# Kernel optimization log

Hardware: AMD Instinct MI355X
Metric: run time of the kernel (lower is better)

Reference implementation:

```python
import jax, jax.numpy as jnp
import numpy as np

N_ATOMS, N_NBH, N_IN, N_FILTERS, N_OUT, N_GAUSS = 10000, 48, 128, 128, 128, 25
R_CUTOFF = 5.0
LOG2 = float(np.log(2.0))


def ssp(v):
    # shifted softplus, the SchNet activation
    return jax.nn.softplus(v) - LOG2


def setup_inputs() -> dict:
    key = jax.random.key(0)
    ks = jax.random.split(key, 10)
    x = jax.random.normal(ks[0], (N_ATOMS, N_IN), dtype=jnp.float32)
    dR = jax.random.uniform(ks[1], (N_ATOMS, N_NBH), dtype=jnp.float32) * 10.0  # distances in [0,10)
    dR_expanded = jax.random.normal(ks[2], (N_ATOMS, N_NBH, N_GAUSS), dtype=jnp.float32)
    pairwise_mask = jnp.ones((N_ATOMS, N_NBH), dtype=jnp.float32)
    neighbors_idx = jax.random.randint(ks[3], (N_ATOMS, N_NBH), 0, N_ATOMS, dtype=jnp.int32)
    s = 1.0 / np.sqrt(N_FILTERS)
    W1 = jax.random.normal(ks[4], (N_GAUSS, N_FILTERS), dtype=jnp.float32) * (1.0 / np.sqrt(N_GAUSS))
    b1 = jnp.zeros((N_FILTERS,), dtype=jnp.float32)
    W2 = jax.random.normal(ks[5], (N_FILTERS, N_FILTERS), dtype=jnp.float32) * s
    b2 = jnp.zeros((N_FILTERS,), dtype=jnp.float32)
    W_in2f = jax.random.normal(ks[6], (N_IN, N_FILTERS), dtype=jnp.float32) * (1.0 / np.sqrt(N_IN))
    W_f2out = jax.random.normal(ks[7], (N_FILTERS, N_OUT), dtype=jnp.float32) * s
    b_f2out = jnp.zeros((N_OUT,), dtype=jnp.float32)
    return {"x": x, "dR": dR, "dR_expanded": dR_expanded, "pairwise_mask": pairwise_mask,
            "neighbors_idx": neighbors_idx, "W1": W1, "b1": b1, "W2": W2, "b2": b2,
            "W_in2f": W_in2f, "W_f2out": W_f2out, "b_f2out": b_f2out}


def reference(x, dR, dR_expanded, pairwise_mask, neighbors_idx,
              W1, b1, W2, b2, W_in2f, W_f2out, b_f2out):
    # FilterNetwork: Dense + ssp + Dense, on Gaussian-smeared distances -> [N, K, F]
    W = jnp.einsum('nkg,gf->nkf', dR_expanded, W1) + b1
    W = jnp.einsum('nkf,fh->nkh', ssp(W), W2) + b2
    # HardCutoff: 1 where within cutoff
    C = (dR <= R_CUTOFF).astype(W.dtype)           # [N, K]
    W = W * C[..., None]
    # in2f (no bias), gather neighbor features
    y = x @ W_in2f                                  # [N, F]
    y = jnp.take(y, neighbors_idx, axis=0)          # [N, K, F] (gather == take_along_axis path)
    # filter-weighted multiply + masked sum aggregation over neighbor axis
    y = y * W
    y = jnp.sum(y * pairwise_mask[..., None], axis=1)  # [N, F]
    # f2out: Linear + shifted softplus
    return ssp(y @ W_f2out + b_f2out)               # [N, n_out]
```

## Files before the change

### kernel.cpp

```cpp
#include <hip/hip_runtime.h>
#include <hip/hip_bf16.h>


#define NA 10000
#define NK 48
#define NF 128
#define HP  136
#define YFP 136
#define GRID_CF 1024

typedef __bf16 bf16x8 __attribute__((ext_vector_type(8)));
typedef float  f32x4  __attribute__((ext_vector_type(4)));

__device__ __forceinline__ unsigned short f2bs(float x) {
    return __builtin_bit_cast(unsigned short, (__bf16)x);
}
__device__ __forceinline__ float bs2f(unsigned short u) {
    return (float)__builtin_bit_cast(__bf16, u);
}
__device__ __forceinline__ float sspf(float v) {
    return fmaxf(v, 0.0f) + __logf(1.0f + __expf(-fabsf(v))) - 0.69314718056f;
}

__global__ __launch_bounds__(256) void in2f_prep(
    const float* __restrict__ x,
    const float* __restrict__ Wi,
    const float* __restrict__ W1,
    const float* __restrict__ W2,
    const float* __restrict__ Wo,
    const float* __restrict__ dRe,
    unsigned short* __restrict__ wsb,
    unsigned short* __restrict__ yfeatb,
    unsigned short* __restrict__ dreb)
{
    const int tid = threadIdx.x;

    if (blockIdx.x >= 301) {
        const float4* src = (const float4*)dRe;
        for (int j = (blockIdx.x - 301) * 256 + tid; j < 3000000; j += 768 * 256) {
            float4 v = src[j];
            int n  = j / 300;
            int rm = j - n * 300;
            int i  = rm * 4;
            int k  = i / 25;
            int g  = i - k * 25;
            unsigned short* dst = dreb + (size_t)n * 1536;
            float vv[4] = {v.x, v.y, v.z, v.w};
            #pragma unroll
            for (int e = 0; e < 4; ++e) {
                dst[k * 32 + g] = f2bs(vv[e]);
                if (++g == 25) {
                    #pragma unroll
                    for (int p = 25; p < 32; ++p) dst[k * 32 + p] = 0;
                    g = 0; ++k;
                }
            }
        }
        return;
    }

    if (blockIdx.x >= 157) {
        int i = (blockIdx.x - 157) * 256 + tid;
        if (i < 4096) {
            int f = i >> 5, g = i & 31;
            wsb[i] = (g < 25) ? f2bs(W1[g * NF + f]) : (unsigned short)0;
        } else if (i < 20480) {
            int j = i - 4096; int h = j >> 7, k = j & 127;
            wsb[i] = f2bs(W2[k * NF + h]);
        } else {
            int j = i - 20480; int f = j >> 7, k = j & 127;
            wsb[i] = f2bs(Wo[k * NF + f]);
        }
        return;
    }

    __shared__ __align__(16) unsigned short s_wi[NF * 136];
    {
        const float4* wi4 = (const float4*)Wi;
        #pragma unroll
        for (int it = 0; it < 16; ++it) {
            int idx4 = it * 256 + tid;
            float4 v = wi4[idx4];
            int i = idx4 >> 5;
            int f = (idx4 & 31) * 4;
            s_wi[(f + 0) * 136 + i] = f2bs(v.x);
            s_wi[(f + 1) * 136 + i] = f2bs(v.y);
            s_wi[(f + 2) * 136 + i] = f2bs(v.z);
            s_wi[(f + 3) * 136 + i] = f2bs(v.w);
        }
    }
    __syncthreads();

    const int w = tid >> 6;
    const int lane = tid & 63;
    const int r = lane & 15;
    const int q = lane >> 4;
    const int m0 = blockIdx.x * 64 + w * 16;
    const int row = m0 + r;
    const bool rv = (row < NA);

    f32x4 acc[8];
    #pragma unroll
    for (int nt = 0; nt < 8; ++nt) { acc[nt][0]=0.f; acc[nt][1]=0.f; acc[nt][2]=0.f; acc[nt][3]=0.f; }

    #pragma unroll
    for (int ks = 0; ks < 4; ++ks) {
        bf16x8 a;
        if (rv) {
            const float4* xp = (const float4*)(x + (size_t)row * NF + ks * 32 + q * 8);
            float4 v0 = xp[0], v1 = xp[1];
            a[0]=(__bf16)v0.x; a[1]=(__bf16)v0.y; a[2]=(__bf16)v0.z; a[3]=(__bf16)v0.w;
            a[4]=(__bf16)v1.x; a[5]=(__bf16)v1.y; a[6]=(__bf16)v1.z; a[7]=(__bf16)v1.w;
        } else {
            #pragma unroll
            for (int j = 0; j < 8; ++j) a[j] = (__bf16)0.0f;
        }
        #pragma unroll
        for (int nt = 0; nt < 8; ++nt) {
            bf16x8 b = *(const bf16x8*)(&s_wi[(nt * 16 + r) * 136 + ks * 32 + q * 8]);
            acc[nt] = __builtin_amdgcn_mfma_f32_16x16x32_bf16(a, b, acc[nt], 0, 0, 0);
        }
    }
    #pragma unroll
    for (int nt = 0; nt < 8; ++nt) {
        #pragma unroll
        for (int reg = 0; reg < 4; ++reg) {
            int orow = m0 + q * 4 + reg;
            if (orow < NA)
                yfeatb[(size_t)orow * NF + nt * 16 + r] = f2bs(acc[nt][reg]);
        }
    }
}

__global__ __launch_bounds__(256, 4) void cfconv_pp(
    const float* __restrict__ dR,
    const float* __restrict__ mask,
    const int*   __restrict__ nbr,
    const float* __restrict__ b1,
    const float* __restrict__ b2,
    const unsigned short* __restrict__ W1T,
    const unsigned short* __restrict__ W2T,
    const unsigned short* __restrict__ dreb,
    const unsigned short* __restrict__ yfeatb,
    float* __restrict__ yout)
{
    __shared__ __align__(16) unsigned short s_H[NK * HP];
    __shared__ __align__(16) unsigned short s_yf[NK * YFP];
    __shared__ float s_cm[NK];

    const int tid = threadIdx.x;
    const int w = tid >> 6;
    const int lane = tid & 63;
    const int r = lane & 15;
    const int q = lane >> 4;
    const int nt0 = w * 2;
    const int kb = tid >> 4;
    const int sp = tid & 15;

    const bf16x8 bfr0 = *(const bf16x8*)(W1T + ((nt0    ) * 16 + r) * 32 + q * 8);
    const bf16x8 bfr1 = *(const bf16x8*)(W1T + ((nt0 + 1) * 16 + r) * 32 + q * 8);
    bf16x8 bw[2][4];
    #pragma unroll
    for (int t = 0; t < 2; ++t)
        #pragma unroll
        for (int ks = 0; ks < 4; ++ks)
            bw[t][ks] = *(const bf16x8*)(W2T + ((nt0 + t) * 16 + r) * NF + ks * 32 + q * 8);
    const float bias1a = b1[nt0 * 16 + r];
    const float bias1b = b1[nt0 * 16 + 16 + r];
    const float bias2a = b2[nt0 * 16 + r];
    const float bias2b = b2[nt0 * 16 + 16 + r];

    bf16x8 g0, g1, g2;
    bf16x8 a0, a1, a2;
    float dv = 10.0f, mv = 0.0f;
    unsigned short hsv[24];

    auto prefetch = [&](int nn) {
        const int nb0 = nbr[nn * NK + kb] * NF;
        const int nb1 = nbr[nn * NK + kb + 16] * NF;
        const int nb2 = nbr[nn * NK + kb + 32] * NF;
        g0 = *(const bf16x8*)(yfeatb + nb0 + sp * 8);
        g1 = *(const bf16x8*)(yfeatb + nb1 + sp * 8);
        g2 = *(const bf16x8*)(yfeatb + nb2 + sp * 8);
        const unsigned short* dn = dreb + (size_t)nn * 1536;
        a0 = *(const bf16x8*)(dn + (     r) * 32 + q * 8);
        a1 = *(const bf16x8*)(dn + (16 + r) * 32 + q * 8);
        a2 = *(const bf16x8*)(dn + (32 + r) * 32 + q * 8);
        if (tid < NK) {
            dv = dR[nn * NK + tid];
            mv = mask[nn * NK + tid];
        }
    };

    auto stage1 = [&]() {
        #pragma unroll
        for (int mt = 0; mt < 3; ++mt) {
            bf16x8 av8 = (mt == 0) ? a0 : (mt == 1) ? a1 : a2;
            f32x4 zf; zf[0]=0.f; zf[1]=0.f; zf[2]=0.f; zf[3]=0.f;
            f32x4 h0v = __builtin_amdgcn_mfma_f32_16x16x32_bf16(av8, bfr0, zf, 0, 0, 0);
            f32x4 h1v = __builtin_amdgcn_mfma_f32_16x16x32_bf16(av8, bfr1, zf, 0, 0, 0);
            #pragma unroll
            for (int reg = 0; reg < 4; ++reg) {
                hsv[mt * 8 + reg]     = f2bs(sspf(h0v[reg] + bias1a));
                hsv[mt * 8 + 4 + reg] = f2bs(sspf(h1v[reg] + bias1b));
            }
        }
    };

    auto ldswrite = [&]() {
        #pragma unroll
        for (int mt = 0; mt < 3; ++mt) {
            #pragma unroll
            for (int reg = 0; reg < 4; ++reg) {
                int k = mt * 16 + q * 4 + reg;
                s_H[k * HP + nt0 * 16 + r]      = hsv[mt * 8 + reg];
                s_H[k * HP + nt0 * 16 + 16 + r] = hsv[mt * 8 + 4 + reg];
            }
        }
        *(bf16x8*)(&s_yf[(kb     ) * YFP + sp * 8]) = g0;
        *(bf16x8*)(&s_yf[(kb + 16) * YFP + sp * 8]) = g1;
        *(bf16x8*)(&s_yf[(kb + 32) * YFP + sp * 8]) = g2;
        if (tid < NK)
            s_cm[tid] = (dv <= 5.0f) ? mv : 0.0f;
    };

    int n = blockIdx.x;
    prefetch(n);
    stage1();
    ldswrite();
    __syncthreads();

    while (true) {
        const int n_next = n + GRID_CF;
        const bool more = (n_next < NA);

        if (more) prefetch(n_next);

        f32x4 acc[3][2];
        #pragma unroll
        for (int mt = 0; mt < 3; ++mt)
            #pragma unroll
            for (int t = 0; t < 2; ++t) { acc[mt][t][0]=0.f; acc[mt][t][1]=0.f; acc[mt][t][2]=0.f; acc[mt][t][3]=0.f; }

        #pragma unroll
        for (int ks = 0; ks < 4; ++ks) {
            #pragma unroll
            for (int mt = 0; mt < 3; ++mt) {
                bf16x8 ah = *(const bf16x8*)(&s_H[(mt * 16 + r) * HP + ks * 32 + q * 8]);
                acc[mt][0] = __builtin_amdgcn_mfma_f32_16x16x32_bf16(ah, bw[0][ks], acc[mt][0], 0, 0, 0);
                acc[mt][1] = __builtin_amdgcn_mfma_f32_16x16x32_bf16(ah, bw[1][ks], acc[mt][1], 0, 0, 0);
            }
        }

        if (more) stage1();

        float part0 = 0.f, part1 = 0.f;
        const int h0 = nt0 * 16 + r;
        #pragma unroll
        for (int mt = 0; mt < 3; ++mt) {
            #pragma unroll
            for (int reg = 0; reg < 4; ++reg) {
                int k = mt * 16 + q * 4 + reg;
                float cmk = s_cm[k];
                part0 += cmk * (acc[mt][0][reg] + bias2a) * bs2f(s_yf[k * YFP + h0]);
                part1 += cmk * (acc[mt][1][reg] + bias2b) * bs2f(s_yf[k * YFP + h0 + 16]);
            }
        }
        part0 += __shfl_xor(part0, 16);
        part0 += __shfl_xor(part0, 32);
        part1 += __shfl_xor(part1, 16);
        part1 += __shfl_xor(part1, 32);
        if (q == 0) {
            yout[(size_t)n * NF + h0]      = part0;
            yout[(size_t)n * NF + h0 + 16] = part1;
        }

        if (!more) break;

        __syncthreads();
        ldswrite();
        __syncthreads();
        n = n_next;
    }
}

__global__ __launch_bounds__(256) void f2out_mfma(
    const unsigned short* __restrict__ WoT,
    const float* __restrict__ bo,
    float* io)
{
    const int tid = threadIdx.x;
    const int w = tid >> 6;
    const int lane = tid & 63;
    const int r = lane & 15;
    const int q = lane >> 4;
    const int m0 = blockIdx.x * 64 + w * 16;
    const int row = m0 + r;
    const bool rv = (row < NA);

    f32x4 acc[8];
    #pragma unroll
    for (int nt = 0; nt < 8; ++nt) { acc[nt][0]=0.f; acc[nt][1]=0.f; acc[nt][2]=0.f; acc[nt][3]=0.f; }

    #pragma unroll
    for (int ks = 0; ks < 4; ++ks) {
        bf16x8 a;
        if (rv) {
            const float4* yp = (const float4*)(io + (size_t)row * NF + ks * 32 + q * 8);
            float4 v0 = yp[0], v1 = yp[1];
            a[0]=(__bf16)v0.x; a[1]=(__bf16)v0.y; a[2]=(__bf16)v0.z; a[3]=(__bf16)v0.w;
            a[4]=(__bf16)v1.x; a[5]=(__bf16)v1.y; a[6]=(__bf16)v1.z; a[7]=(__bf16)v1.w;
        } else {
            #pragma unroll
            for (int j = 0; j < 8; ++j) a[j] = (__bf16)0.0f;
        }
        #pragma unroll
        for (int nt = 0; nt < 8; ++nt) {
            bf16x8 b = *(const bf16x8*)(WoT + (nt * 16 + r) * NF + ks * 32 + q * 8);
            acc[nt] = __builtin_amdgcn_mfma_f32_16x16x32_bf16(a, b, acc[nt], 0, 0, 0);
        }
    }
    #pragma unroll
    for (int nt = 0; nt < 8; ++nt) {
        float bia = bo[nt * 16 + r];
        #pragma unroll
        for (int reg = 0; reg < 4; ++reg) {
            int orow = m0 + q * 4 + reg;
            if (orow < NA)
                io[(size_t)orow * NF + nt * 16 + r] = sspf(acc[nt][reg] + bia);
        }
    }
}

extern "C" void kernel_launch(void* const* d_in, const int* in_sizes, int n_in,
                              void* d_out, int out_size, void* d_ws, size_t ws_size,
                              hipStream_t stream)
{
    const float* x    = (const float*)d_in[0];
    const float* dR   = (const float*)d_in[1];
    const float* dRe  = (const float*)d_in[2];
    const float* mask = (const float*)d_in[3];
    const int*   nbr  = (const int*)d_in[4];
    const float* W1   = (const float*)d_in[5];
    const float* b1   = (const float*)d_in[6];
    const float* W2   = (const float*)d_in[7];
    const float* b2   = (const float*)d_in[8];
    const float* Wi2f = (const float*)d_in[9];
    const float* Wf2o = (const float*)d_in[10];
    const float* bf2o = (const float*)d_in[11];
    float* out = (float*)d_out;

    unsigned short* wsb = (unsigned short*)d_ws;
    unsigned short* W1T    = wsb;
    unsigned short* W2T    = wsb + 4096;
    unsigned short* WoT    = wsb + 20480;
    unsigned short* yfeatb = wsb + 36864;
    unsigned short* dreb   = wsb + 1316864;

    in2f_prep<<<1069, 256, 0, stream>>>(x, Wi2f, W1, W2, Wf2o, dRe,
                                        wsb, yfeatb, dreb);
    cfconv_pp<<<GRID_CF, 256, 0, stream>>>(dR, mask, nbr, b1, b2,
                                           W1T, W2T, dreb, yfeatb, out);
    f2out_mfma<<<157, 256, 0, stream>>>(WoT, bf2o, out);
}
```

Baseline: 209.5 us.

## Fuse prep, cfconv and f2out into one persistent kernel with grid barriers

Merges the three launches (weight/dR_expanded conversion plus in2f GEMM, the cfconv filter/aggregation loop, and the f2out GEMM) into a single persistent kernel. Phases are separated by software grid barriers built on atomic counters, and the grid is sized from the occupancy query (up to 6 blocks per CU × 256). The aim is to remove launch gaps and tail effects between kernels. In exchange it adds barrier spin costs, a memset launch, and a deadlock risk if the grid is not fully co-resident; the old three-kernel path is kept as a fallback when the workspace is too small.

```diff
diff --git a/kernel.cpp b/kernel.cpp
--- a/kernel.cpp
+++ b/kernel.cpp
@@ -7,7 +7,6 @@
 #define NF 128
 #define HP  136
 #define YFP 136
-#define GRID_CF 1024
 
 typedef __bf16 bf16x8 __attribute__((ext_vector_type(8)));
 typedef float  f32x4  __attribute__((ext_vector_type(4)));
@@ -22,7 +21,311 @@
     return fmaxf(v, 0.0f) + __logf(1.0f + __expf(-fabsf(v))) - 0.69314718056f;
 }
 
-__global__ __launch_bounds__(256) void in2f_prep(
+__device__ __forceinline__ void gridbar(unsigned int* cnt, unsigned int target) {
+    __syncthreads();
+    if (threadIdx.x == 0) {
+        __threadfence();
+        __hip_atomic_fetch_add(cnt, 1u, __ATOMIC_ACQ_REL, __HIP_MEMORY_SCOPE_AGENT);
+        unsigned int guard = 0;
+        while (__hip_atomic_load(cnt, __ATOMIC_ACQUIRE, __HIP_MEMORY_SCOPE_AGENT) < target) {
+            if (++guard > 100000000u) break;
+            __builtin_amdgcn_s_sleep(2);
+        }
+        __threadfence();
+    }
+    __syncthreads();
+}
+
+__global__ __launch_bounds__(256, 4) void cfconv_fused(
+    const float* __restrict__ x,
+    const float* __restrict__ dR,
+    const float* __restrict__ dRe,
+    const float* __restrict__ mask,
+    const int*   __restrict__ nbr,
+    const float* __restrict__ b1,
+    const float* __restrict__ b2,
+    const float* __restrict__ W1,
+    const float* __restrict__ W2,
+    const float* __restrict__ Wi,
+    const float* __restrict__ Wo,
+    const float* __restrict__ bf2o,
+    unsigned short* __restrict__ wsb,
+    unsigned short* __restrict__ yfeatb,
+    unsigned short* __restrict__ dreb,
+    unsigned int* bar,
+    float* __restrict__ out)
+{
+    __shared__ __align__(16) unsigned short s_H[NK * HP];
+    __shared__ __align__(16) unsigned short s_yf[NK * YFP];
+    __shared__ float s_cm[NK];
+
+    const int tid  = threadIdx.x;
+    const int bid  = blockIdx.x;
+    const int nblk = gridDim.x;
+    const unsigned int NB = (unsigned int)nblk;
+
+    const int w = tid >> 6;
+    const int lane = tid & 63;
+    const int r = lane & 15;
+    const int q = lane >> 4;
+    const int nt0 = w * 2;
+    const int kb = tid >> 4;
+    const int sp = tid & 15;
+
+    const unsigned short* W1T = wsb;
+    const unsigned short* W2T = wsb + 4096;
+    const unsigned short* WiT = wsb + 20480;
+    const unsigned short* WoT = wsb + 36864;
+
+    {
+        int i = bid * 256 + tid;
+        if (i < 4096) {
+            int f = i >> 5, g = i & 31;
+            wsb[i] = (g < 25) ? f2bs(W1[g * NF + f]) : (unsigned short)0;
+        } else if (i < 20480) {
+            int j = i - 4096; int h = j >> 7, k = j & 127;
+            wsb[i] = f2bs(W2[k * NF + h]);
+        } else if (i < 36864) {
+            int j = i - 20480; int f = j >> 7, k = j & 127;
+            wsb[i] = f2bs(Wi[k * NF + f]);
+        } else if (i < 53248) {
+            int j = i - 36864; int f = j >> 7, k = j & 127;
+            wsb[i] = f2bs(Wo[k * NF + f]);
+        }
+
+        const float4* src = (const float4*)dRe;
+        for (int j = bid * 256 + tid; j < 3000000; j += nblk * 256) {
+            float4 v = src[j];
+            int n  = j / 300;
+            int rm = j - n * 300;
+            int i2 = rm * 4;
+            int k  = i2 / 25;
+            int g  = i2 - k * 25;
+            unsigned short* dst = dreb + (size_t)n * 1536;
+            float vv[4] = {v.x, v.y, v.z, v.w};
+            #pragma unroll
+            for (int e = 0; e < 4; ++e) {
+                dst[k * 32 + g] = f2bs(vv[e]);
+                if (++g == 25) {
+                    #pragma unroll
+                    for (int p = 25; p < 32; ++p) dst[k * 32 + p] = 0;
+                    g = 0; ++k;
+                }
+            }
+        }
+    }
+    gridbar(bar + 0, NB);
+
+    for (int tile = bid; tile < 157; tile += nblk) {
+        const int m0 = tile * 64 + w * 16;
+        const int row = m0 + r;
+        const bool rv = (row < NA);
+
+        f32x4 acc[8];
+        #pragma unroll
+        for (int nt = 0; nt < 8; ++nt) { acc[nt][0]=0.f; acc[nt][1]=0.f; acc[nt][2]=0.f; acc[nt][3]=0.f; }
+
+        #pragma unroll
+        for (int ks = 0; ks < 4; ++ks) {
+            bf16x8 a;
+            if (rv) {
+                const float4* xp = (const float4*)(x + (size_t)row * NF + ks * 32 + q * 8);
+                float4 v0 = xp[0], v1 = xp[1];
+                a[0]=(__bf16)v0.x; a[1]=(__bf16)v0.y; a[2]=(__bf16)v0.z; a[3]=(__bf16)v0.w;
+                a[4]=(__bf16)v1.x; a[5]=(__bf16)v1.y; a[6]=(__bf16)v1.z; a[7]=(__bf16)v1.w;
+            } else {
+                #pragma unroll
+                for (int j = 0; j < 8; ++j) a[j] = (__bf16)0.0f;
+            }
+            #pragma unroll
+            for (int nt = 0; nt < 8; ++nt) {
+                bf16x8 b = *(const bf16x8*)(WiT + (nt * 16 + r) * NF + ks * 32 + q * 8);
+                acc[nt] = __builtin_amdgcn_mfma_f32_16x16x32_bf16(a, b, acc[nt], 0, 0, 0);
+            }
+        }
+        #pragma unroll
+        for (int nt = 0; nt < 8; ++nt) {
+            #pragma unroll
+            for (int reg = 0; reg < 4; ++reg) {
+                int orow = m0 + q * 4 + reg;
+                if (orow < NA)
+                    yfeatb[(size_t)orow * NF + nt * 16 + r] = f2bs(acc[nt][reg]);
+            }
+        }
+    }
+    gridbar(bar + 1, NB);
+
+    {
+        const bf16x8 bfr0 = *(const bf16x8*)(W1T + ((nt0    ) * 16 + r) * 32 + q * 8);
+        const bf16x8 bfr1 = *(const bf16x8*)(W1T + ((nt0 + 1) * 16 + r) * 32 + q * 8);
+        bf16x8 bw[2][4];
+        #pragma unroll
+        for (int t = 0; t < 2; ++t)
+            #pragma unroll
+            for (int ks = 0; ks < 4; ++ks)
+                bw[t][ks] = *(const bf16x8*)(W2T + ((nt0 + t) * 16 + r) * NF + ks * 32 + q * 8);
+        const float bias1a = b1[nt0 * 16 + r];
+        const float bias1b = b1[nt0 * 16 + 16 + r];
+        const float bias2a = b2[nt0 * 16 + r];
+        const float bias2b = b2[nt0 * 16 + 16 + r];
+
+        bf16x8 g0, g1, g2;
+        bf16x8 a0, a1, a2;
+        float dv = 10.0f, mv = 0.0f;
+        unsigned short hsv[24];
+
+        auto prefetch = [&](int nn) {
+            const int nb0 = nbr[nn * NK + kb] * NF;
+            const int nb1 = nbr[nn * NK + kb + 16] * NF;
+            const int nb2 = nbr[nn * NK + kb + 32] * NF;
+            g0 = *(const bf16x8*)(yfeatb + nb0 + sp * 8);
+            g1 = *(const bf16x8*)(yfeatb + nb1 + sp * 8);
+            g2 = *(const bf16x8*)(yfeatb + nb2 + sp * 8);
+            const unsigned short* dn = dreb + (size_t)nn * 1536;
+            a0 = *(const bf16x8*)(dn + (     r) * 32 + q * 8);
+            a1 = *(const bf16x8*)(dn + (16 + r) * 32 + q * 8);
+            a2 = *(const bf16x8*)(dn + (32 + r) * 32 + q * 8);
+            if (tid < NK) {
+                dv = dR[nn * NK + tid];
+                mv = mask[nn * NK + tid];
+            }
+        };
+
+        auto stage1 = [&]() {
+            #pragma unroll
+            for (int mt = 0; mt < 3; ++mt) {
+                bf16x8 av8 = (mt == 0) ? a0 : (mt == 1) ? a1 : a2;
+                f32x4 zf; zf[0]=0.f; zf[1]=0.f; zf[2]=0.f; zf[3]=0.f;
+                f32x4 h0v = __builtin_amdgcn_mfma_f32_16x16x32_bf16(av8, bfr0, zf, 0, 0, 0);
+                f32x4 h1v = __builtin_amdgcn_mfma_f32_16x16x32_bf16(av8, bfr1, zf, 0, 0, 0);
+                #pragma unroll
+                for (int reg = 0; reg < 4; ++reg) {
+                    hsv[mt * 8 + reg]     = f2bs(sspf(h0v[reg] + bias1a));
+                    hsv[mt * 8 + 4 + reg] = f2bs(sspf(h1v[reg] + bias1b));
+                }
+            }
+        };
+
+        auto ldswrite = [&]() {
+            #pragma unroll
+            for (int mt = 0; mt < 3; ++mt) {
+                #pragma unroll
+                for (int reg = 0; reg < 4; ++reg) {
+                    int k = mt * 16 + q * 4 + reg;
+                    s_H[k * HP + nt0 * 16 + r]      = hsv[mt * 8 + reg];
+                    s_H[k * HP + nt0 * 16 + 16 + r] = hsv[mt * 8 + 4 + reg];
+                }
+            }
+            *(bf16x8*)(&s_yf[(kb     ) * YFP + sp * 8]) = g0;
+            *(bf16x8*)(&s_yf[(kb + 16) * YFP + sp * 8]) = g1;
+            *(bf16x8*)(&s_yf[(kb + 32) * YFP + sp * 8]) = g2;
+            if (tid < NK)
+                s_cm[tid] = (dv <= 5.0f) ? mv : 0.0f;
+        };
+
+        int n = bid;
+        prefetch(n);
+        stage1();
+        ldswrite();
+        __syncthreads();
+
+        while (true) {
+            const int n_next = n + nblk;
+            const bool more = (n_next < NA);
+
+            if (more) prefetch(n_next);
+
+            f32x4 acc[3][2];
+            #pragma unroll
+            for (int mt = 0; mt < 3; ++mt)
+                #pragma unroll
+                for (int t = 0; t < 2; ++t) { acc[mt][t][0]=0.f; acc[mt][t][1]=0.f; acc[mt][t][2]=0.f; acc[mt][t][3]=0.f; }
+
+            #pragma unroll
+            for (int ks = 0; ks < 4; ++ks) {
+                #pragma unroll
+                for (int mt = 0; mt < 3; ++mt) {
+                    bf16x8 ah = *(const bf16x8*)(&s_H[(mt * 16 + r) * HP + ks * 32 + q * 8]);
+                    acc[mt][0] = __builtin_amdgcn_mfma_f32_16x16x32_bf16(ah, bw[0][ks], acc[mt][0], 0, 0, 0);
+                    acc[mt][1] = __builtin_amdgcn_mfma_f32_16x16x32_bf16(ah, bw[1][ks], acc[mt][1], 0, 0, 0);
+                }
+            }
+
+            if (more) stage1();
+
+            float part0 = 0.f, part1 = 0.f;
+            const int h0 = nt0 * 16 + r;
+            #pragma unroll
+            for (int mt = 0; mt < 3; ++mt) {
+                #pragma unroll
+                for (int reg = 0; reg < 4; ++reg) {
+                    int k = mt * 16 + q * 4 + reg;
+                    float cmk = s_cm[k];
+                    part0 += cmk * (acc[mt][0][reg] + bias2a) * bs2f(s_yf[k * YFP + h0]);
+                    part1 += cmk * (acc[mt][1][reg] + bias2b) * bs2f(s_yf[k * YFP + h0 + 16]);
+                }
+            }
+            part0 += __shfl_xor(part0, 16);
+            part0 += __shfl_xor(part0, 32);
+            part1 += __shfl_xor(part1, 16);
+            part1 += __shfl_xor(part1, 32);
+            if (q == 0) {
+                out[(size_t)n * NF + h0]      = part0;
+                out[(size_t)n * NF + h0 + 16] = part1;
+            }
+
+            if (!more) break;
+
+            __syncthreads();
+            ldswrite();
+            __syncthreads();
+            n = n_next;
+        }
+    }
+    gridbar(bar + 2, NB);
+
+    for (int tile = bid; tile < 157; tile += nblk) {
+        const int m0 = tile * 64 + w * 16;
+        const int row = m0 + r;
+        const bool rv = (row < NA);
+
+        f32x4 acc[8];
+        #pragma unroll
+        for (int nt = 0; nt < 8; ++nt) { acc[nt][0]=0.f; acc[nt][1]=0.f; acc[nt][2]=0.f; acc[nt][3]=0.f; }
+
+        #pragma unroll
+        for (int ks = 0; ks < 4; ++ks) {
+            bf16x8 a;
+            if (rv) {
+                const float4* yp = (const float4*)(out + (size_t)row * NF + ks * 32 + q * 8);
+                float4 v0 = yp[0], v1 = yp[1];
+                a[0]=(__bf16)v0.x; a[1]=(__bf16)v0.y; a[2]=(__bf16)v0.z; a[3]=(__bf16)v0.w;
+                a[4]=(__bf16)v1.x; a[5]=(__bf16)v1.y; a[6]=(__bf16)v1.z; a[7]=(__bf16)v1.w;
+            } else {
+                #pragma unroll
+                for (int j = 0; j < 8; ++j) a[j] = (__bf16)0.0f;
+            }
+            #pragma unroll
+            for (int nt = 0; nt < 8; ++nt) {
+                bf16x8 b = *(const bf16x8*)(WoT + (nt * 16 + r) * NF + ks * 32 + q * 8);
+                acc[nt] = __builtin_amdgcn_mfma_f32_16x16x32_bf16(a, b, acc[nt], 0, 0, 0);
+            }
+        }
+        #pragma unroll
+        for (int nt = 0; nt < 8; ++nt) {
+            float bia = bf2o[nt * 16 + r];
+            #pragma unroll
+            for (int reg = 0; reg < 4; ++reg) {
+                int orow = m0 + q * 4 + reg;
+                if (orow < NA)
+                    out[(size_t)orow * NF + nt * 16 + r] = sspf(acc[nt][reg] + bia);
+            }
+        }
+    }
+}
+
+
+__global__ __launch_bounds__(256) void in2f_prep_fb(
     const float* __restrict__ x,
     const float* __restrict__ Wi,
     const float* __restrict__ W1,
@@ -132,7 +435,7 @@
     }
 }
 
-__global__ __launch_bounds__(256, 4) void cfconv_pp(
+__global__ __launch_bounds__(256, 4) void cfconv_pp_fb(
     const float* __restrict__ dR,
     const float* __restrict__ mask,
     const int*   __restrict__ nbr,
@@ -170,8 +473,7 @@
     const float bias2a = b2[nt0 * 16 + r];
     const float bias2b = b2[nt0 * 16 + 16 + r];
 
-    bf16x8 g0, g1, g2;
-    bf16x8 a0, a1, a2;
+    bf16x8 g0, g1, g2, a0, a1, a2;
     float dv = 10.0f, mv = 0.0f;
     unsigned short hsv[24];
 
@@ -186,12 +488,8 @@
         a0 = *(const bf16x8*)(dn + (     r) * 32 + q * 8);
         a1 = *(const bf16x8*)(dn + (16 + r) * 32 + q * 8);
         a2 = *(const bf16x8*)(dn + (32 + r) * 32 + q * 8);
-        if (tid < NK) {
-            dv = dR[nn * NK + tid];
-            mv = mask[nn * NK + tid];
-        }
+        if (tid < NK) { dv = dR[nn * NK + tid]; mv = mask[nn * NK + tid]; }
     };
-
     auto stage1 = [&]() {
         #pragma unroll
         for (int mt = 0; mt < 3; ++mt) {
@@ -206,34 +504,28 @@
             }
         }
     };
-
     auto ldswrite = [&]() {
         #pragma unroll
-        for (int mt = 0; mt < 3; ++mt) {
+        for (int mt = 0; mt < 3; ++mt)
             #pragma unroll
             for (int reg = 0; reg < 4; ++reg) {
                 int k = mt * 16 + q * 4 + reg;
                 s_H[k * HP + nt0 * 16 + r]      = hsv[mt * 8 + reg];
                 s_H[k * HP + nt0 * 16 + 16 + r] = hsv[mt * 8 + 4 + reg];
             }
-        }
         *(bf16x8*)(&s_yf[(kb     ) * YFP + sp * 8]) = g0;
         *(bf16x8*)(&s_yf[(kb + 16) * YFP + sp * 8]) = g1;
         *(bf16x8*)(&s_yf[(kb + 32) * YFP + sp * 8]) = g2;
-        if (tid < NK)
-            s_cm[tid] = (dv <= 5.0f) ? mv : 0.0f;
+        if (tid < NK) s_cm[tid] = (dv <= 5.0f) ? mv : 0.0f;
     };
 
     int n = blockIdx.x;
-    prefetch(n);
-    stage1();
-    ldswrite();
+    prefetch(n); stage1(); ldswrite();
     __syncthreads();
 
     while (true) {
-        const int n_next = n + GRID_CF;
+        const int n_next = n + 1024;
         const bool more = (n_next < NA);
-
         if (more) prefetch(n_next);
 
         f32x4 acc[3][2];
@@ -243,21 +535,20 @@
             for (int t = 0; t < 2; ++t) { acc[mt][t][0]=0.f; acc[mt][t][1]=0.f; acc[mt][t][2]=0.f; acc[mt][t][3]=0.f; }
 
         #pragma unroll
-        for (int ks = 0; ks < 4; ++ks) {
+        for (int ks = 0; ks < 4; ++ks)
             #pragma unroll
             for (int mt = 0; mt < 3; ++mt) {
                 bf16x8 ah = *(const bf16x8*)(&s_H[(mt * 16 + r) * HP + ks * 32 + q * 8]);
                 acc[mt][0] = __builtin_amdgcn_mfma_f32_16x16x32_bf16(ah, bw[0][ks], acc[mt][0], 0, 0, 0);
                 acc[mt][1] = __builtin_amdgcn_mfma_f32_16x16x32_bf16(ah, bw[1][ks], acc[mt][1], 0, 0, 0);
             }
-        }
 
         if (more) stage1();
 
         float part0 = 0.f, part1 = 0.f;
         const int h0 = nt0 * 16 + r;
         #pragma unroll
-        for (int mt = 0; mt < 3; ++mt) {
+        for (int mt = 0; mt < 3; ++mt)
             #pragma unroll
             for (int reg = 0; reg < 4; ++reg) {
                 int k = mt * 16 + q * 4 + reg;
@@ -265,7 +556,6 @@
                 part0 += cmk * (acc[mt][0][reg] + bias2a) * bs2f(s_yf[k * YFP + h0]);
                 part1 += cmk * (acc[mt][1][reg] + bias2b) * bs2f(s_yf[k * YFP + h0 + 16]);
             }
-        }
         part0 += __shfl_xor(part0, 16);
         part0 += __shfl_xor(part0, 32);
         part1 += __shfl_xor(part1, 16);
@@ -276,7 +566,6 @@
         }
 
         if (!more) break;
-
         __syncthreads();
         ldswrite();
         __syncthreads();
@@ -284,7 +573,7 @@
     }
 }
 
-__global__ __launch_bounds__(256) void f2out_mfma(
+__global__ __launch_bounds__(256) void f2out_mfma_fb(
     const unsigned short* __restrict__ WoT,
     const float* __restrict__ bo,
     float* io)
@@ -351,15 +640,36 @@
     float* out = (float*)d_out;
 
     unsigned short* wsb = (unsigned short*)d_ws;
-    unsigned short* W1T    = wsb;
-    unsigned short* W2T    = wsb + 4096;
-    unsigned short* WoT    = wsb + 20480;
-    unsigned short* yfeatb = wsb + 36864;
-    unsigned short* dreb   = wsb + 1316864;
-
-    in2f_prep<<<1069, 256, 0, stream>>>(x, Wi2f, W1, W2, Wf2o, dRe,
-                                        wsb, yfeatb, dreb);
-    cfconv_pp<<<GRID_CF, 256, 0, stream>>>(dR, mask, nbr, b1, b2,
-                                           W1T, W2T, dreb, yfeatb, out);
-    f2out_mfma<<<157, 256, 0, stream>>>(WoT, bf2o, out);
-}
+
+    bool fused_ok = ws_size >= 33386752ULL;
+    int occ = 0;
+    if (fused_ok) {
+        if (hipOccupancyMaxActiveBlocksPerMultiprocessor(&occ, cfconv_fused, 256, 0) != hipSuccess)
+            occ = 0;
+        if (occ < 1) fused_ok = false;
+    }
+
+    if (fused_ok) {
+        unsigned short* yfb  = wsb + 53248;
+        unsigned short* dreb = wsb + 1333248;
+        unsigned int*   bar  = (unsigned int*)(wsb + 16693248);
+        int bpc  = occ > 6 ? 6 : occ;
+        int grid = bpc * 256;
+        if (grid > 1536) grid = 1536;
+        hipMemsetAsync(bar, 0, 128, stream);
+        cfconv_fused<<<grid, 256, 0, stream>>>(x, dR, dRe, mask, nbr, b1, b2,
+                                               W1, W2, Wi2f, Wf2o, bf2o,
+                                               wsb, yfb, dreb, bar, out);
+    } else {
+        unsigned short* W1T    = wsb;
+        unsigned short* W2T    = wsb + 4096;
+        unsigned short* WoT    = wsb + 20480;
+        unsigned short* yfeatb = wsb + 36864;
+        unsigned short* dreb   = wsb + 1316864;
+        in2f_prep_fb<<<1069, 256, 0, stream>>>(x, Wi2f, W1, W2, Wf2o, dRe,
+                                               wsb, yfeatb, dreb);
+        cfconv_pp_fb<<<1024, 256, 0, stream>>>(dR, mask, nbr, b1, b2,
+                                               W1T, W2T, dreb, yfeatb, out);
+        f2out_mfma_fb<<<157, 256, 0, stream>>>(WoT, bf2o, out);
+    }
+}
```

Measured after the change: 571.0 us. 173% more time.

## Read fp32 Gaussian expansion directly in cfconv instead of bf16 pre-pass

Applied to the files above, without the earlier changes.

Drops the separate pass that converted dR_expanded to a padded bf16 buffer. The cfconv kernel now loads the fp32 values straight from the input and converts them to bf16 in registers. Lanes with q==3 load only the 25th element and zero-fill the rest of the padded K. Weight transposes move into their own small kernel, and in2f reads a pre-transposed Wi from global memory instead of building it in LDS. This removes about 48MB of write-plus-reread traffic, at the cost of unaligned fp32 loads inside the main kernel and one extra kernel launch.

```diff
diff --git a/kernel.cpp b/kernel.cpp
--- a/kernel.cpp
+++ b/kernel.cpp
@@ -22,75 +22,35 @@
     return fmaxf(v, 0.0f) + __logf(1.0f + __expf(-fabsf(v))) - 0.69314718056f;
 }
 
-__global__ __launch_bounds__(256) void in2f_prep(
-    const float* __restrict__ x,
-    const float* __restrict__ Wi,
+__global__ __launch_bounds__(256) void prep_weights(
     const float* __restrict__ W1,
     const float* __restrict__ W2,
+    const float* __restrict__ Wi,
     const float* __restrict__ Wo,
-    const float* __restrict__ dRe,
-    unsigned short* __restrict__ wsb,
-    unsigned short* __restrict__ yfeatb,
-    unsigned short* __restrict__ dreb)
+    unsigned short* __restrict__ wsb)
+{
+    int i = blockIdx.x * 256 + threadIdx.x;
+    if (i < 4096) {
+        int f = i >> 5, g = i & 31;
+        wsb[i] = (g < 25) ? f2bs(W1[g * NF + f]) : (unsigned short)0;
+    } else if (i < 20480) {
+        int j = i - 4096; int h = j >> 7, k = j & 127;
+        wsb[i] = f2bs(W2[k * NF + h]);
+    } else if (i < 36864) {
+        int j = i - 20480; int f = j >> 7, k = j & 127;
+        wsb[i] = f2bs(Wi[k * NF + f]);
+    } else if (i < 53248) {
+        int j = i - 36864; int f = j >> 7, k = j & 127;
+        wsb[i] = f2bs(Wo[k * NF + f]);
+    }
+}
+
+__global__ __launch_bounds__(256) void in2f_mfma(
+    const float* __restrict__ x,
+    const unsigned short* __restrict__ WiT,
+    unsigned short* __restrict__ yfeatb)
 {
     const int tid = threadIdx.x;
-
-    if (blockIdx.x >= 301) {
-        const float4* src = (const float4*)dRe;
-        for (int j = (blockIdx.x - 301) * 256 + tid; j < 3000000; j += 768 * 256) {
-            float4 v = src[j];
-            int n  = j / 300;
-            int rm = j - n * 300;
-            int i  = rm * 4;
-            int k  = i / 25;
-            int g  = i - k * 25;
-            unsigned short* dst = dreb + (size_t)n * 1536;
-            float vv[4] = {v.x, v.y, v.z, v.w};
-            #pragma unroll
-            for (int e = 0; e < 4; ++e) {
-                dst[k * 32 + g] = f2bs(vv[e]);
-                if (++g == 25) {
-                    #pragma unroll
-                    for (int p = 25; p < 32; ++p) dst[k * 32 + p] = 0;
-                    g = 0; ++k;
-                }
-            }
-        }
-        return;
-    }
-
-    if (blockIdx.x >= 157) {
-        int i = (blockIdx.x - 157) * 256 + tid;
-        if (i < 4096) {
-            int f = i >> 5, g = i & 31;
-            wsb[i] = (g < 25) ? f2bs(W1[g * NF + f]) : (unsigned short)0;
-        } else if (i < 20480) {
-            int j = i - 4096; int h = j >> 7, k = j & 127;
-            wsb[i] = f2bs(W2[k * NF + h]);
-        } else {
-            int j = i - 20480; int f = j >> 7, k = j & 127;
-            wsb[i] = f2bs(Wo[k * NF + f]);
-        }
-        return;
-    }
-
-    __shared__ __align__(16) unsigned short s_wi[NF * 136];
-    {
-        const float4* wi4 = (const float4*)Wi;
-        #pragma unroll
-        for (int it = 0; it < 16; ++it) {
-            int idx4 = it * 256 + tid;
-            float4 v = wi4[idx4];
-            int i = idx4 >> 5;
-            int f = (idx4 & 31) * 4;
-            s_wi[(f + 0) * 136 + i] = f2bs(v.x);
-            s_wi[(f + 1) * 136 + i] = f2bs(v.y);
-            s_wi[(f + 2) * 136 + i] = f2bs(v.z);
-            s_wi[(f + 3) * 136 + i] = f2bs(v.w);
-        }
-    }
-    __syncthreads();
-
     const int w = tid >> 6;
     const int lane = tid & 63;
     const int r = lane & 15;
@@ -117,7 +77,7 @@
         }
         #pragma unroll
         for (int nt = 0; nt < 8; ++nt) {
-            bf16x8 b = *(const bf16x8*)(&s_wi[(nt * 16 + r) * 136 + ks * 32 + q * 8]);
+            bf16x8 b = *(const bf16x8*)(WiT + (nt * 16 + r) * NF + ks * 32 + q * 8);
             acc[nt] = __builtin_amdgcn_mfma_f32_16x16x32_bf16(a, b, acc[nt], 0, 0, 0);
         }
     }
@@ -132,15 +92,15 @@
     }
 }
 
-__global__ __launch_bounds__(256, 4) void cfconv_pp(
+__global__ __launch_bounds__(256, 4) void cfconv_ppd(
     const float* __restrict__ dR,
+    const float* __restrict__ dRe,
     const float* __restrict__ mask,
     const int*   __restrict__ nbr,
     const float* __restrict__ b1,
     const float* __restrict__ b2,
     const unsigned short* __restrict__ W1T,
     const unsigned short* __restrict__ W2T,
-    const unsigned short* __restrict__ dreb,
     const unsigned short* __restrict__ yfeatb,
     float* __restrict__ yout)
 {
@@ -171,7 +131,7 @@
     const float bias2b = b2[nt0 * 16 + 16 + r];
 
     bf16x8 g0, g1, g2;
-    bf16x8 a0, a1, a2;
+    float  fv[3][8];
     float dv = 10.0f, mv = 0.0f;
     unsigned short hsv[24];
 
@@ -182,10 +142,16 @@
         g0 = *(const bf16x8*)(yfeatb + nb0 + sp * 8);
         g1 = *(const bf16x8*)(yfeatb + nb1 + sp * 8);
         g2 = *(const bf16x8*)(yfeatb + nb2 + sp * 8);
-        const unsigned short* dn = dreb + (size_t)nn * 1536;
-        a0 = *(const bf16x8*)(dn + (     r) * 32 + q * 8);
-        a1 = *(const bf16x8*)(dn + (16 + r) * 32 + q * 8);
-        a2 = *(const bf16x8*)(dn + (32 + r) * 32 + q * 8);
+        const float* dre_n = dRe + (size_t)nn * (NK * 25);
+        if (q < 3) {
+            #pragma unroll
+            for (int mt = 0; mt < 3; ++mt)
+                __builtin_memcpy(fv[mt], dre_n + (mt * 16 + r) * 25 + q * 8, 32);
+        } else {
+            #pragma unroll
+            for (int mt = 0; mt < 3; ++mt)
+                fv[mt][0] = dre_n[(mt * 16 + r) * 25 + 24];
+        }
         if (tid < NK) {
             dv = dR[nn * NK + tid];
             mv = mask[nn * NK + tid];
@@ -195,7 +161,15 @@
     auto stage1 = [&]() {
         #pragma unroll
         for (int mt = 0; mt < 3; ++mt) {
-            bf16x8 av8 = (mt == 0) ? a0 : (mt == 1) ? a1 : a2;
+            bf16x8 av8;
+            if (q < 3) {
+                #pragma unroll
+                for (int j = 0; j < 8; ++j) av8[j] = (__bf16)fv[mt][j];
+            } else {
+                av8[0] = (__bf16)fv[mt][0];
+                #pragma unroll
+                for (int j = 1; j < 8; ++j) av8[j] = (__bf16)0.0f;
+            }
             f32x4 zf; zf[0]=0.f; zf[1]=0.f; zf[2]=0.f; zf[3]=0.f;
             f32x4 h0v = __builtin_amdgcn_mfma_f32_16x16x32_bf16(av8, bfr0, zf, 0, 0, 0);
             f32x4 h1v = __builtin_amdgcn_mfma_f32_16x16x32_bf16(av8, bfr1, zf, 0, 0, 0);
@@ -353,13 +327,13 @@
     unsigned short* wsb = (unsigned short*)d_ws;
     unsigned short* W1T    = wsb;
     unsigned short* W2T    = wsb + 4096;
-    unsigned short* WoT    = wsb + 20480;
-    unsigned short* yfeatb = wsb + 36864;
-    unsigned short* dreb   = wsb + 1316864;
-
-    in2f_prep<<<1069, 256, 0, stream>>>(x, Wi2f, W1, W2, Wf2o, dRe,
-                                        wsb, yfeatb, dreb);
-    cfconv_pp<<<GRID_CF, 256, 0, stream>>>(dR, mask, nbr, b1, b2,
-                                           W1T, W2T, dreb, yfeatb, out);
+    unsigned short* WiT    = wsb + 20480;
+    unsigned short* WoT    = wsb + 36864;
+    unsigned short* yfeatb = wsb + 53248;
+
+    prep_weights<<<208, 256, 0, stream>>>(W1, W2, Wi2f, Wf2o, wsb);
+    in2f_mfma<<<157, 256, 0, stream>>>(x, WiT, yfeatb);
+    cfconv_ppd<<<GRID_CF, 256, 0, stream>>>(dR, dRe, mask, nbr, b1, b2,
+                                            W1T, W2T, yfeatb, out);
     f2out_mfma<<<157, 256, 0, stream>>>(WoT, bf2o, out);
 }
```

After: 298.5 us. 42.5% more time.
